# Kernel tuning notes

Hardware: AMD Instinct MI355X
Metric: run time of the kernel (lower is better)

## Reference

```python
import jax, jax.numpy as jnp
import numpy as np

ATT_PROP = 2  # config['att_prop']
NEG_BIAS = 1e23


def _bucket(d):
    # standard coref-style distance bucketing into 10 buckets
    d = jnp.abs(d)
    return jnp.where(d <= 4, d,
           jnp.where(d <= 7, 5,
           jnp.where(d <= 15, 6,
           jnp.where(d <= 31, 7,
           jnp.where(d <= 63, 8, 9))))).astype(jnp.int32)


def setup_inputs() -> dict:
    key = jax.random.key(0)
    ks = jax.random.split(key, 12)
    B, N, M, D, H = 2, 1024, 2048, 512, 64
    scale = 0.02  # init_weights_std

    update = jax.random.normal(ks[0], (B, N, D), jnp.float32)
    span_begin = jnp.sort(jax.random.randint(ks[1], (B, N), 0, 2000), axis=-1).astype(jnp.int32)
    span_end = (span_begin + jax.random.randint(ks[2], (B, N), 0, 10)).astype(jnp.int32)
    square_mask = jnp.ones((B, N, N), jnp.float32)
    cand_span_vecs = jax.random.normal(ks[3], (B, M, D), jnp.float32)
    # unique prune indices per batch (a pruned span maps to one candidate slot)
    prune_indices_hoi = jnp.stack([
        jnp.sort(jax.random.permutation(jax.random.fold_in(ks[4], b), M)[:N])
        for b in range(B)]).astype(jnp.int32)
    span_lengths = jnp.array([900, 1024], dtype=jnp.int32)

    W_left = jax.random.normal(ks[5], (D, H), jnp.float32) * scale
    W_right = jax.random.normal(ks[6], (D, H), jnp.float32) * scale
    b_h = jnp.zeros((H,), jnp.float32)
    dist_emb = jax.random.normal(ks[7], (10, H), jnp.float32) * scale
    v_out = jax.random.normal(ks[8], (H,), jnp.float32) * scale
    b_out = jnp.zeros((), jnp.float32)
    W_gate = jax.random.normal(ks[9], (2 * D, D), jnp.float32) * scale
    b_gate = jnp.zeros((D,), jnp.float32)

    return dict(update=update, square_mask=square_mask, cand_span_vecs=cand_span_vecs,
                span_begin=span_begin, span_end=span_end,
                prune_indices_hoi=prune_indices_hoi, span_lengths=span_lengths,
                W_left=W_left, W_right=W_right, b_h=b_h, dist_emb=dist_emb,
                v_out=v_out, b_out=b_out, W_gate=W_gate, b_gate=b_gate)


def reference(update, square_mask, cand_span_vecs, span_begin, span_end,
              prune_indices_hoi, span_lengths, W_left, W_right, b_h,
              dist_emb, v_out, b_out, W_gate, b_gate):
    B, N, D = update.shape
    # pairwise distance features are iteration-invariant: precompute once
    dist = dist_emb[_bucket(span_begin[:, :, None] - span_begin[:, None, :])]  # [B,N,N,H]
    bias = -(1.0 - square_mask) * NEG_BIAS  # [B,N,N]

    for _ in range(ATT_PROP):
        left = update @ W_left    # [B,N,H]
        right = update @ W_right  # [B,N,H]
        h = jax.nn.relu(left[:, :, None, :] + right[:, None, :, :] + dist + b_h)  # [B,N,N,H]
        scores = jnp.einsum('bijh,h->bij', h, v_out) + b_out  # [B,N,N]
        probs = jax.nn.softmax(scores + bias, axis=-1)
        ctxt = jnp.einsum('bij,bjd->bid', probs, update)  # [B,N,D]
        g = jax.nn.sigmoid(jnp.concatenate([update, ctxt], axis=-1) @ W_gate + b_gate)
        update = g * update + (1.0 - g) * ctxt

    # overwrite_spans_hoi: scatter first span_lengths[b] updated vectors back
    valid = jnp.arange(N) < span_lengths[:, None]  # [B,N]

    def scatter_one(cand, idx, upd, m):
        cur = cand[idx]  # [N,D]
        vals = jnp.where(m[:, None], upd, cur)  # invalid rows write back original
        return cand.at[idx].set(vals)

    cand_new = jax.vmap(scatter_one)(cand_span_vecs, prune_indices_hoi, update, valid)
    return cand_new, update
```

## Files before the change

### kernel.cpp

```cpp
#include <hip/hip_runtime.h>
#include <cstdint>

#define NB 2
#define NN 1024
#define MM 2048
#define DD 512
#define HH 64
#define ST 68
#define STB 72

typedef __attribute__((ext_vector_type(8))) short bf16x8;
typedef __attribute__((ext_vector_type(4))) float f32x4;

__device__ inline ushort f2bf(float x) {
  union { float f; uint32_t u; } v; v.f = x;
  uint32_t u = v.u;
  u += 0x7FFF + ((u >> 16) & 1);
  return (ushort)(u >> 16);
}
__device__ inline float bflo(uint32_t d) { return __uint_as_float(d << 16); }
__device__ inline float bfhi(uint32_t d) { return __uint_as_float(d & 0xFFFF0000u); }

#define GLDS(gp, lp) \
  __builtin_amdgcn_global_load_lds( \
      (const __attribute__((address_space(1))) void*)(gp), \
      (__attribute__((address_space(3))) void*)(lp), 16, 0, 0)

__global__ __launch_bounds__(256) void prep_kernel(
    const float* __restrict__ Wg, ushort* __restrict__ WgT,
    const float* __restrict__ update, ushort* __restrict__ Ubf0,
    ushort* __restrict__ UT, const float* __restrict__ cand,
    float* __restrict__ out, const float* __restrict__ Wl,
    const float* __restrict__ Wr, float* __restrict__ left,
    ushort* __restrict__ right_bf) {
  __shared__ __align__(16) char smem[16640];
  const int bid = blockIdx.x;
  const int tid = threadIdx.x;
  const int tx = tid & 15, ty = tid >> 4;

  if (bid < 384) {
    const float* in;
    ushort* out_row;
    ushort* out_T;
    int R, C, r0, c0;
    if (bid < 128) {
      in = Wg; out_row = nullptr; out_T = WgT;
      R = 2 * DD; C = DD; r0 = (bid >> 3) * 64; c0 = (bid & 7) * 64;
    } else {
      const int t = bid - 128, b = t >> 7, rem = t & 127;
      in = update + (size_t)b * NN * DD;
      out_row = Ubf0 + (size_t)b * NN * DD;
      out_T = UT + (size_t)b * DD * NN;
      R = NN; C = DD; r0 = (rem >> 3) * 64; c0 = (rem & 7) * 64;
    }
    float (*tile)[65] = (float(*)[65])smem;
#pragma unroll
    for (int p = 0; p < 4; ++p) {
      const int r = ty + p * 16;
      const float4 v = *(const float4*)&in[(size_t)(r0 + r) * C + c0 + tx * 4];
      tile[r][tx * 4 + 0] = v.x; tile[r][tx * 4 + 1] = v.y;
      tile[r][tx * 4 + 2] = v.z; tile[r][tx * 4 + 3] = v.w;
      if (out_row) {
        ushort4 o = make_ushort4(f2bf(v.x), f2bf(v.y), f2bf(v.z), f2bf(v.w));
        *(ushort4*)&out_row[(size_t)(r0 + r) * C + c0 + tx * 4] = o;
      }
    }
    __syncthreads();
#pragma unroll
    for (int p = 0; p < 4; ++p) {
      const int rr = ty + p * 16;
      ushort4 o;
      o.x = f2bf(tile[tx * 4 + 0][rr]);
      o.y = f2bf(tile[tx * 4 + 1][rr]);
      o.z = f2bf(tile[tx * 4 + 2][rr]);
      o.w = f2bf(tile[tx * 4 + 3][rr]);
      *(ushort4*)&out_T[(size_t)(c0 + rr) * R + r0 + tx * 4] = o;
    }
    __syncthreads();
  }

  {
    float (*u)[DD] = (float(*)[DD])smem;
    const float4* Uv = (const float4*)(update + (size_t)bid * 4 * DD);
    float4* uv = (float4*)&u[0][0];
#pragma unroll
    for (int t = 0; t < 2; ++t) uv[tid + t * 256] = Uv[tid + t * 256];
    __syncthreads();
    const int h = tid & 63;
    const int isR = (tid >> 6) & 1;
    const int rsel = tid >> 7;
    const float* __restrict__ W = isR ? Wr : Wl;
    float acc[2] = {0.f, 0.f};
    for (int k0 = 0; k0 < DD; k0 += 4) {
      float w0 = W[(k0 + 0) * HH + h];
      float w1 = W[(k0 + 1) * HH + h];
      float w2 = W[(k0 + 2) * HH + h];
      float w3 = W[(k0 + 3) * HH + h];
#pragma unroll
      for (int r = 0; r < 2; ++r) {
        float4 u4 = *(const float4*)&u[rsel + r * 2][k0];
        acc[r] = fmaf(u4.w, w3, fmaf(u4.z, w2, fmaf(u4.y, w1, fmaf(u4.x, w0, acc[r]))));
      }
    }
    if (isR) {
#pragma unroll
      for (int r = 0; r < 2; ++r)
        right_bf[(size_t)(bid * 4 + rsel + r * 2) * HH + h] = f2bf(acc[r]);
    } else {
#pragma unroll
      for (int r = 0; r < 2; ++r)
        left[(size_t)(bid * 4 + rsel + r * 2) * HH + h] = acc[r];
    }
  }

  {
    const float4* c4 = (const float4*)cand;
    float4* o4 = (float4*)out;
    for (int idx = bid * 256 + tid; idx < NB * MM * DD / 4; idx += 512 * 256)
      o4[idx] = c4[idx];
  }
}

__global__ __launch_bounds__(256) void lr_kernel(
    const float* __restrict__ U, const float* __restrict__ Wl,
    const float* __restrict__ Wr, float* __restrict__ left,
    ushort* __restrict__ right_bf) {
  __shared__ float u[4][DD];
  const int bid = blockIdx.x;
  const int tid = threadIdx.x;
  const float4* Uv = (const float4*)(U + (size_t)bid * 4 * DD);
  float4* uv = (float4*)&u[0][0];
#pragma unroll
  for (int t = 0; t < 2; ++t) uv[tid + t * 256] = Uv[tid + t * 256];
  __syncthreads();
  const int h = tid & 63;
  const int isR = (tid >> 6) & 1;
  const int rsel = tid >> 7;
  const float* __restrict__ W = isR ? Wr : Wl;
  float acc[2] = {0.f, 0.f};
  for (int k0 = 0; k0 < DD; k0 += 4) {
    float w0 = W[(k0 + 0) * HH + h];
    float w1 = W[(k0 + 1) * HH + h];
    float w2 = W[(k0 + 2) * HH + h];
    float w3 = W[(k0 + 3) * HH + h];
#pragma unroll
    for (int r = 0; r < 2; ++r) {
      float4 u4 = *(const float4*)&u[rsel + r * 2][k0];
      acc[r] = fmaf(u4.w, w3, fmaf(u4.z, w2, fmaf(u4.y, w1, fmaf(u4.x, w0, acc[r]))));
    }
  }
  if (isR) {
#pragma unroll
    for (int r = 0; r < 2; ++r)
      right_bf[(size_t)(bid * 4 + rsel + r * 2) * HH + h] = f2bf(acc[r]);
  } else {
#pragma unroll
    for (int r = 0; r < 2; ++r)
      left[(size_t)(bid * 4 + rsel + r * 2) * HH + h] = acc[r];
  }
}

__global__ __launch_bounds__(256) void score_softmax(
    const float* __restrict__ left, const ushort* __restrict__ right_bf,
    const int* __restrict__ span_begin, const float* __restrict__ mask,
    const float* __restrict__ dist_emb, const float* __restrict__ b_h,
    const float* __restrict__ v_out, ushort* __restrict__ probs_bf) {
  __shared__ ushort Rt[128][STB];
  __shared__ ushort LDb[4][10][STB];
  __shared__ float Dbh[10][ST];
  __shared__ float Lt[4][ST];
  __shared__ float Sc[4][NN];
  __shared__ int sbj[NN];
  const int b = blockIdx.y;
  const int r0 = blockIdx.x * 4;
  const int tid = threadIdx.x;
  const int wave = tid >> 6, lane = tid & 63;
  const int row = r0 + wave;

  for (int f = tid; f < 160; f += 256) {
    int bk = f >> 4, h4 = f & 15;
    float4 d = *(const float4*)&dist_emb[bk * HH + h4 * 4];
    float4 bh = *(const float4*)&b_h[h4 * 4];
    d.x += bh.x; d.y += bh.y; d.z += bh.z; d.w += bh.w;
    *(float4*)&Dbh[bk][h4 * 4] = d;
  }
  if (tid < 64) {
    int r = tid >> 4, h4 = tid & 15;
    *(float4*)&Lt[r][h4 * 4] =
        *(const float4*)&left[((size_t)b * NN + r0 + r) * HH + h4 * 4];
  }
  for (int t = tid; t < NN; t += 256) sbj[t] = span_begin[b * NN + t];
  __syncthreads();
  for (int f = tid; f < 2560; f += 256) {
    int i = f / 640;
    int rem = f - i * 640;
    int bk = rem >> 6, h = rem & 63;
    LDb[i][bk][h] = f2bf(Lt[i][h] + Dbh[bk][h]);
  }
  float4 vr[16];
#pragma unroll
  for (int hq = 0; hq < 16; ++hq) vr[hq] = *(const float4*)&v_out[hq * 4];
  const int my_sbi = span_begin[(size_t)b * NN + row];
  const float* maskrow = mask + ((size_t)b * NN + row) * NN;

#pragma unroll 1
  for (int c = 0; c < 8; ++c) {
    __syncthreads();
#pragma unroll
    for (int t = 0; t < 4; ++t) {
      const int f = tid + t * 256;
      const int r = f >> 3, u8 = f & 7;
      *(bf16x8*)&Rt[r][u8 * 8] =
          *(const bf16x8*)&right_bf[((size_t)b * NN + c * 128 + r) * HH + u8 * 8];
    }
    __syncthreads();
#pragma unroll 1
    for (int half = 0; half < 2; ++half) {
      const int j = c * 128 + half * 64 + lane;
      int d = sbj[j] - my_sbi;
      d = d < 0 ? -d : d;
      const int bk =
          d <= 4 ? d : (d <= 7 ? 5 : (d <= 15 ? 6 : (d <= 31 ? 7 : (d <= 63 ? 8 : 9))));
      const ushort* zp = &LDb[wave][bk][0];
      const ushort* rp = &Rt[half * 64 + lane][0];
      float acc0 = 0.f, acc1 = 0.f;
#pragma unroll
      for (int oct = 0; oct < 8; oct += 2) {
        {
          const uint4 zd = *(const uint4*)&zp[oct * 8];
          const uint4 rd = *(const uint4*)&rp[oct * 8];
          const float4 v0 = vr[2 * oct], v1 = vr[2 * oct + 1];
          acc0 = fmaf(fmaxf(bflo(zd.x) + bflo(rd.x), 0.f), v0.x, acc0);
          acc0 = fmaf(fmaxf(bfhi(zd.x) + bfhi(rd.x), 0.f), v0.y, acc0);
          acc0 = fmaf(fmaxf(bflo(zd.y) + bflo(rd.y), 0.f), v0.z, acc0);
          acc0 = fmaf(fmaxf(bfhi(zd.y) + bfhi(rd.y), 0.f), v0.w, acc0);
          acc0 = fmaf(fmaxf(bflo(zd.z) + bflo(rd.z), 0.f), v1.x, acc0);
          acc0 = fmaf(fmaxf(bfhi(zd.z) + bfhi(rd.z), 0.f), v1.y, acc0);
          acc0 = fmaf(fmaxf(bflo(zd.w) + bflo(rd.w), 0.f), v1.z, acc0);
          acc0 = fmaf(fmaxf(bfhi(zd.w) + bfhi(rd.w), 0.f), v1.w, acc0);
        }
        {
          const uint4 zd = *(const uint4*)&zp[(oct + 1) * 8];
          const uint4 rd = *(const uint4*)&rp[(oct + 1) * 8];
          const float4 v0 = vr[2 * oct + 2], v1 = vr[2 * oct + 3];
          acc1 = fmaf(fmaxf(bflo(zd.x) + bflo(rd.x), 0.f), v0.x, acc1);
          acc1 = fmaf(fmaxf(bfhi(zd.x) + bfhi(rd.x), 0.f), v0.y, acc1);
          acc1 = fmaf(fmaxf(bflo(zd.y) + bflo(rd.y), 0.f), v0.z, acc1);
          acc1 = fmaf(fmaxf(bfhi(zd.y) + bfhi(rd.y), 0.f), v0.w, acc1);
          acc1 = fmaf(fmaxf(bflo(zd.z) + bflo(rd.z), 0.f), v1.x, acc1);
          acc1 = fmaf(fmaxf(bfhi(zd.z) + bfhi(rd.z), 0.f), v1.y, acc1);
          acc1 = fmaf(fmaxf(bflo(zd.w) + bflo(rd.w), 0.f), v1.z, acc1);
          acc1 = fmaf(fmaxf(bfhi(zd.w) + bfhi(rd.w), 0.f), v1.w, acc1);
        }
      }
      const float mval = maskrow[j];
      Sc[wave][j] = (acc0 + acc1) - (1.0f - mval) * 1e23f;
    }
  }
  float mx = -3.0e38f;
#pragma unroll
  for (int c = 0; c < 16; ++c) mx = fmaxf(mx, Sc[wave][c * 64 + lane]);
#pragma unroll
  for (int off = 32; off; off >>= 1) mx = fmaxf(mx, __shfl_xor(mx, off));
  float sum = 0.f;
#pragma unroll
  for (int c = 0; c < 16; ++c) {
    const float e = __expf(Sc[wave][c * 64 + lane] - mx);
    Sc[wave][c * 64 + lane] = e;
    sum += e;
  }
#pragma unroll
  for (int off = 32; off; off >>= 1) sum += __shfl_xor(sum, off);
  const float inv = 1.0f / sum;
  ushort* prow = probs_bf + ((size_t)b * NN + row) * NN;
#pragma unroll
  for (int c = 0; c < 16; ++c)
    prow[c * 64 + lane] = f2bf(Sc[wave][c * 64 + lane] * inv);
}

__global__ __launch_bounds__(256) void gemm_ctxt_mfma(
    const ushort* __restrict__ Pbf, const ushort* __restrict__ UT,
    ushort* __restrict__ Cbf) {
  __shared__ ushort As[32 * 128];
  __shared__ ushort Bs[64 * 128];
  const int b = blockIdx.z;
  const int m0 = blockIdx.y * 32, n0 = blockIdx.x * 64;
  const int tid = threadIdx.x;
  const int lane = tid & 63, wave = tid >> 6;
  const int wm = (wave >> 1) * 16, wn = (wave & 1) * 32;
  const ushort* Ab = Pbf + (size_t)b * NN * NN;
  const ushort* Bb = UT + (size_t)b * DD * NN;
  f32x4 acc[2] = {};
  const int fm = lane & 15, quad = lane >> 4;
  for (int k0 = 0; k0 < NN; k0 += 128) {
#pragma unroll
    for (int t = 0; t < 2; ++t) {
      const int idx = tid + t * 256;
      const int r = idx >> 4, c16 = idx & 15;
      const int g = c16 ^ (r & 15);
      GLDS(Ab + (size_t)(m0 + r) * NN + k0 + g * 8, As + idx * 8);
    }
#pragma unroll
    for (int t = 0; t < 4; ++t) {
      const int idx = tid + t * 256;
      const int r = idx >> 4, c16 = idx & 15;
      const int g = c16 ^ (r & 15);
      GLDS(Bb + (size_t)(n0 + r) * NN + k0 + g * 8, Bs + idx * 8);
    }
    __syncthreads();
#pragma unroll
    for (int s = 0; s < 4; ++s) {
      bf16x8 af, bfr[2];
      {
        const int row = wm + fm;
        const int c16 = (s * 4 + quad) ^ (row & 15);
        af = *(const bf16x8*)&As[row * 128 + c16 * 8];
      }
#pragma unroll
      for (int tn = 0; tn < 2; ++tn) {
        const int row = wn + tn * 16 + fm;
        const int c16 = (s * 4 + quad) ^ (row & 15);
        bfr[tn] = *(const bf16x8*)&Bs[row * 128 + c16 * 8];
      }
#pragma unroll
      for (int tn = 0; tn < 2; ++tn)
        acc[tn] = __builtin_amdgcn_mfma_f32_16x16x32_bf16(af, bfr[tn], acc[tn], 0, 0, 0);
    }
    __syncthreads();
  }
#pragma unroll
  for (int tn = 0; tn < 2; ++tn) {
    const int col = n0 + wn + tn * 16 + fm;
#pragma unroll
    for (int r = 0; r < 4; ++r) {
      const int row = m0 + wm + quad * 4 + r;
      Cbf[(size_t)b * NN * DD + (size_t)row * DD + col] = f2bf(acc[tn][r]);
    }
  }
}

__global__ __launch_bounds__(256) void gemm_gate_mfma(
    const ushort* __restrict__ Ubf, const ushort* __restrict__ Cbf,
    const ushort* __restrict__ WgT, const float* __restrict__ bg,
    const float* __restrict__ Uf, float* __restrict__ Uout,
    ushort* __restrict__ UbfOut, ushort* __restrict__ UTOut,
    const int* __restrict__ prune, const int* __restrict__ span_len,
    float* __restrict__ out_cand, int final_it) {
  __shared__ ushort As[32 * 128];
  __shared__ ushort Bs[64 * 128];
  __shared__ ushort Tt[32][66];
  const int b = blockIdx.z;
  const int m0 = blockIdx.y * 32, n0 = blockIdx.x * 64;
  const int tid = threadIdx.x;
  const int lane = tid & 63, wave = tid >> 6;
  const int wm = (wave >> 1) * 16, wn = (wave & 1) * 32;
  f32x4 acc[2] = {};
  const int fm = lane & 15, quad = lane >> 4;
  for (int k0 = 0; k0 < 2 * DD; k0 += 128) {
    const ushort* Abase = (k0 < DD) ? (Ubf + (size_t)b * NN * DD)
                                    : (Cbf + (size_t)b * NN * DD);
    const int kc = k0 & (DD - 1);
#pragma unroll
    for (int t = 0; t < 2; ++t) {
      const int idx = tid + t * 256;
      const int r = idx >> 4, c16 = idx & 15;
      const int g = c16 ^ (r & 15);
      GLDS(Abase + (size_t)(m0 + r) * DD + kc + g * 8, As + idx * 8);
    }
#pragma unroll
    for (int t = 0; t < 4; ++t) {
      const int idx = tid + t * 256;
      const int r = idx >> 4, c16 = idx & 15;
      const int g = c16 ^ (r & 15);
      GLDS(WgT + (size_t)(n0 + r) * (2 * DD) + k0 + g * 8, Bs + idx * 8);
    }
    __syncthreads();
#pragma unroll
    for (int s = 0; s < 4; ++s) {
      bf16x8 af, bfr[2];
      {
        const int row = wm + fm;
        const int c16 = (s * 4 + quad) ^ (row & 15);
        af = *(const bf16x8*)&As[row * 128 + c16 * 8];
      }
#pragma unroll
      for (int tn = 0; tn < 2; ++tn) {
        const int row = wn + tn * 16 + fm;
        const int c16 = (s * 4 + quad) ^ (row & 15);
        bfr[tn] = *(const bf16x8*)&Bs[row * 128 + c16 * 8];
      }
#pragma unroll
      for (int tn = 0; tn < 2; ++tn)
        acc[tn] = __builtin_amdgcn_mfma_f32_16x16x32_bf16(af, bfr[tn], acc[tn], 0, 0, 0);
    }
    __syncthreads();
  }
  const int slen = span_len[b];
#pragma unroll
  for (int tn = 0; tn < 2; ++tn) {
    const int cl = wn + tn * 16 + fm;
    const int col = n0 + cl;
    const float bgv = bg[col];
#pragma unroll
    for (int r = 0; r < 4; ++r) {
      const int rl = wm + quad * 4 + r;
      const int row = m0 + rl;
      const size_t off = (size_t)b * NN * DD + (size_t)row * DD + col;
      const float g = 1.f / (1.f + __expf(-(acc[tn][r] + bgv)));
      const float cv = __uint_as_float(((uint32_t)Cbf[off]) << 16);
      const float o = g * Uf[off] + (1.f - g) * cv;
      Uout[off] = o;
      if (final_it) {
        if (row < slen) {
          const int dst = prune[b * NN + row];
          out_cand[((size_t)b * MM + dst) * DD + col] = o;
        }
      } else {
        const ushort ob = f2bf(o);
        UbfOut[off] = ob;
        Tt[rl][cl] = ob;
      }
    }
  }
  if (!final_it) {
    __syncthreads();
#pragma unroll
    for (int p = 0; p < 2; ++p) {
      const int cl = (tid >> 3) + p * 32;
      const int rl = (tid & 7) * 4;
      ushort4 o;
      o.x = Tt[rl + 0][cl]; o.y = Tt[rl + 1][cl];
      o.z = Tt[rl + 2][cl]; o.w = Tt[rl + 3][cl];
      *(ushort4*)&UTOut[((size_t)b * DD + n0 + cl) * NN + m0 + rl] = o;
    }
  }
}

extern "C" void kernel_launch(void* const* d_in, const int* in_sizes, int n_in,
                              void* d_out, int out_size, void* d_ws, size_t ws_size,
                              hipStream_t stream) {
  const float* update = (const float*)d_in[0];
  const float* mask = (const float*)d_in[1];
  const float* cand = (const float*)d_in[2];
  const int* span_begin = (const int*)d_in[3];
  const int* prune = (const int*)d_in[5];
  const int* span_len = (const int*)d_in[6];
  const float* Wl = (const float*)d_in[7];
  const float* Wr = (const float*)d_in[8];
  const float* b_h = (const float*)d_in[9];
  const float* dist_emb = (const float*)d_in[10];
  const float* v_out = (const float*)d_in[11];
  const float* Wg = (const float*)d_in[13];
  const float* b_gate = (const float*)d_in[14];

  char* w = (char*)d_ws;
  float* left = (float*)w;        w += (size_t)NB * NN * HH * 4;
  ushort* right_bf = (ushort*)w;  w += (size_t)NB * NN * HH * 2;
  ushort* probs_bf = (ushort*)w;  w += (size_t)NB * NN * NN * 2;
  ushort* ctxt_bf = (ushort*)w;   w += (size_t)NB * NN * DD * 2;
  float* upd1 = (float*)w;        w += (size_t)NB * NN * DD * 4;
  ushort* Ubf0 = (ushort*)w;      w += (size_t)NB * NN * DD * 2;
  ushort* Ubf1 = (ushort*)w;      w += (size_t)NB * NN * DD * 2;
  ushort* UT = (ushort*)w;        w += (size_t)NB * NN * DD * 2;
  ushort* WgT = (ushort*)w;       w += (size_t)2 * DD * DD * 2;

  float* out = (float*)d_out;
  float* out_upd = out + (size_t)NB * MM * DD;

  prep_kernel<<<512, 256, 0, stream>>>(Wg, WgT, update, Ubf0, UT, cand, out,
                                       Wl, Wr, left, right_bf);
  score_softmax<<<dim3(NN / 4, NB), 256, 0, stream>>>(
      left, right_bf, span_begin, mask, dist_emb, b_h, v_out, probs_bf);
  gemm_ctxt_mfma<<<dim3(8, 32, NB), 256, 0, stream>>>(probs_bf, UT, ctxt_bf);
  gemm_gate_mfma<<<dim3(8, 32, NB), 256, 0, stream>>>(
      Ubf0, ctxt_bf, WgT, b_gate, update, upd1, Ubf1, UT,
      prune, span_len, out, 0);
  lr_kernel<<<512, 256, 0, stream>>>(upd1, Wl, Wr, left, right_bf);
  score_softmax<<<dim3(NN / 4, NB), 256, 0, stream>>>(
      left, right_bf, span_begin, mask, dist_emb, b_h, v_out, probs_bf);
  gemm_ctxt_mfma<<<dim3(8, 32, NB), 256, 0, stream>>>(probs_bf, UT, ctxt_bf);
  gemm_gate_mfma<<<dim3(8, 32, NB), 256, 0, stream>>>(
      Ubf1, ctxt_bf, WgT, b_gate, upd1, out_upd, nullptr, nullptr,
      prune, span_len, out, 1);
}
```

Measured before the change: 222.0 us.

## Double-buffer shared tiles in score, ctxt and gate kernels to overlap loads

The score kernel now prefetches the next 128-row chunk of right_bf into registers while computing the current chunk, then writes it into a second LDS buffer. This removes one barrier per chunk, and the mask values are loaded up front. The ctxt and gate MFMA GEMMs use ping-pong LDS buffers so the async global-to-LDS copy of tile k+1 is issued before computing tile k, which also drops the trailing barrier. In exchange, LDS use doubles and register pressure rises, which may lower occupancy.

```diff
diff --git a/kernel.cpp b/kernel.cpp
--- a/kernel.cpp
+++ b/kernel.cpp
@@ -165,7 +165,7 @@
     const int* __restrict__ span_begin, const float* __restrict__ mask,
     const float* __restrict__ dist_emb, const float* __restrict__ b_h,
     const float* __restrict__ v_out, ushort* __restrict__ probs_bf) {
-  __shared__ ushort Rt[128][STB];
+  __shared__ ushort Rt[2][128][STB];
   __shared__ ushort LDb[4][10][STB];
   __shared__ float Dbh[10][ST];
   __shared__ float Lt[4][ST];
@@ -202,19 +202,35 @@
   for (int hq = 0; hq < 16; ++hq) vr[hq] = *(const float4*)&v_out[hq * 4];
   const int my_sbi = span_begin[(size_t)b * NN + row];
   const float* maskrow = mask + ((size_t)b * NN + row) * NN;
+  const ushort* rbase = right_bf + (size_t)b * NN * HH;
+
+  bf16x8 stg[4];
+#pragma unroll
+  for (int t = 0; t < 4; ++t) {
+    const int f = tid + t * 256;
+    stg[t] = *(const bf16x8*)&rbase[(size_t)(f >> 3) * HH + (f & 7) * 8];
+  }
+#pragma unroll
+  for (int t = 0; t < 4; ++t) {
+    const int f = tid + t * 256;
+    *(bf16x8*)&Rt[0][f >> 3][(f & 7) * 8] = stg[t];
+  }
 
 #pragma unroll 1
   for (int c = 0; c < 8; ++c) {
-    __syncthreads();
-#pragma unroll
-    for (int t = 0; t < 4; ++t) {
-      const int f = tid + t * 256;
-      const int r = f >> 3, u8 = f & 7;
-      *(bf16x8*)&Rt[r][u8 * 8] =
-          *(const bf16x8*)&right_bf[((size_t)b * NN + c * 128 + r) * HH + u8 * 8];
-    }
-    __syncthreads();
-#pragma unroll 1
+    if (c + 1 < 8) {
+#pragma unroll
+      for (int t = 0; t < 4; ++t) {
+        const int f = tid + t * 256;
+        stg[t] = *(const bf16x8*)&rbase[(size_t)((c + 1) * 128 + (f >> 3)) * HH +
+                                        (f & 7) * 8];
+      }
+    }
+    __syncthreads();
+    float mv[2];
+    mv[0] = maskrow[c * 128 + lane];
+    mv[1] = maskrow[c * 128 + 64 + lane];
+#pragma unroll
     for (int half = 0; half < 2; ++half) {
       const int j = c * 128 + half * 64 + lane;
       int d = sbj[j] - my_sbi;
@@ -222,7 +238,7 @@
       const int bk =
           d <= 4 ? d : (d <= 7 ? 5 : (d <= 15 ? 6 : (d <= 31 ? 7 : (d <= 63 ? 8 : 9))));
       const ushort* zp = &LDb[wave][bk][0];
-      const ushort* rp = &Rt[half * 64 + lane][0];
+      const ushort* rp = &Rt[c & 1][half * 64 + lane][0];
       float acc0 = 0.f, acc1 = 0.f;
 #pragma unroll
       for (int oct = 0; oct < 8; oct += 2) {
@@ -253,8 +269,14 @@
           acc1 = fmaf(fmaxf(bfhi(zd.w) + bfhi(rd.w), 0.f), v1.w, acc1);
         }
       }
-      const float mval = maskrow[j];
-      Sc[wave][j] = (acc0 + acc1) - (1.0f - mval) * 1e23f;
+      Sc[wave][j] = (acc0 + acc1) - (1.0f - mv[half]) * 1e23f;
+    }
+    if (c + 1 < 8) {
+#pragma unroll
+      for (int t = 0; t < 4; ++t) {
+        const int f = tid + t * 256;
+        *(bf16x8*)&Rt[(c + 1) & 1][f >> 3][(f & 7) * 8] = stg[t];
+      }
     }
   }
   float mx = -3.0e38f;
@@ -281,8 +303,8 @@
 __global__ __launch_bounds__(256) void gemm_ctxt_mfma(
     const ushort* __restrict__ Pbf, const ushort* __restrict__ UT,
     ushort* __restrict__ Cbf) {
-  __shared__ ushort As[32 * 128];
-  __shared__ ushort Bs[64 * 128];
+  __shared__ ushort As[2][32 * 128];
+  __shared__ ushort Bs[2][64 * 128];
   const int b = blockIdx.z;
   const int m0 = blockIdx.y * 32, n0 = blockIdx.x * 64;
   const int tid = threadIdx.x;
@@ -292,41 +314,47 @@
   const ushort* Bb = UT + (size_t)b * DD * NN;
   f32x4 acc[2] = {};
   const int fm = lane & 15, quad = lane >> 4;
-  for (int k0 = 0; k0 < NN; k0 += 128) {
-#pragma unroll
-    for (int t = 0; t < 2; ++t) {
-      const int idx = tid + t * 256;
-      const int r = idx >> 4, c16 = idx & 15;
-      const int g = c16 ^ (r & 15);
-      GLDS(Ab + (size_t)(m0 + r) * NN + k0 + g * 8, As + idx * 8);
-    }
-#pragma unroll
-    for (int t = 0; t < 4; ++t) {
-      const int idx = tid + t * 256;
-      const int r = idx >> 4, c16 = idx & 15;
-      const int g = c16 ^ (r & 15);
-      GLDS(Bb + (size_t)(n0 + r) * NN + k0 + g * 8, Bs + idx * 8);
-    }
-    __syncthreads();
+
+#define CTXT_STAGE(buf, kk)                                                  \
+  do {                                                                       \
+    _Pragma("unroll") for (int t = 0; t < 2; ++t) {                          \
+      const int idx = tid + t * 256;                                         \
+      const int r = idx >> 4, c16 = idx & 15;                                \
+      const int g = c16 ^ (r & 15);                                          \
+      GLDS(Ab + (size_t)(m0 + r) * NN + (kk) + g * 8, &As[buf][idx * 8]);    \
+    }                                                                        \
+    _Pragma("unroll") for (int t = 0; t < 4; ++t) {                          \
+      const int idx = tid + t * 256;                                         \
+      const int r = idx >> 4, c16 = idx & 15;                                \
+      const int g = c16 ^ (r & 15);                                          \
+      GLDS(Bb + (size_t)(n0 + r) * NN + (kk) + g * 8, &Bs[buf][idx * 8]);    \
+    }                                                                        \
+  } while (0)
+
+  CTXT_STAGE(0, 0);
+#pragma unroll 1
+  for (int k = 0; k < 8; ++k) {
+    __syncthreads();
+    if (k + 1 < 8) CTXT_STAGE((k + 1) & 1, (k + 1) * 128);
+    const int cur = k & 1;
 #pragma unroll
     for (int s = 0; s < 4; ++s) {
       bf16x8 af, bfr[2];
       {
         const int row = wm + fm;
         const int c16 = (s * 4 + quad) ^ (row & 15);
-        af = *(const bf16x8*)&As[row * 128 + c16 * 8];
+        af = *(const bf16x8*)&As[cur][row * 128 + c16 * 8];
       }
 #pragma unroll
       for (int tn = 0; tn < 2; ++tn) {
         const int row = wn + tn * 16 + fm;
         const int c16 = (s * 4 + quad) ^ (row & 15);
-        bfr[tn] = *(const bf16x8*)&Bs[row * 128 + c16 * 8];
+        bfr[tn] = *(const bf16x8*)&Bs[cur][row * 128 + c16 * 8];
       }
 #pragma unroll
       for (int tn = 0; tn < 2; ++tn)
         acc[tn] = __builtin_amdgcn_mfma_f32_16x16x32_bf16(af, bfr[tn], acc[tn], 0, 0, 0);
     }
-    __syncthreads();
   }
 #pragma unroll
   for (int tn = 0; tn < 2; ++tn) {
@@ -346,8 +374,8 @@
     ushort* __restrict__ UbfOut, ushort* __restrict__ UTOut,
     const int* __restrict__ prune, const int* __restrict__ span_len,
     float* __restrict__ out_cand, int final_it) {
-  __shared__ ushort As[32 * 128];
-  __shared__ ushort Bs[64 * 128];
+  __shared__ ushort As[2][32 * 128];
+  __shared__ ushort Bs[2][64 * 128];
   __shared__ ushort Tt[32][66];
   const int b = blockIdx.z;
   const int m0 = blockIdx.y * 32, n0 = blockIdx.x * 64;
@@ -356,44 +384,51 @@
   const int wm = (wave >> 1) * 16, wn = (wave & 1) * 32;
   f32x4 acc[2] = {};
   const int fm = lane & 15, quad = lane >> 4;
-  for (int k0 = 0; k0 < 2 * DD; k0 += 128) {
-    const ushort* Abase = (k0 < DD) ? (Ubf + (size_t)b * NN * DD)
-                                    : (Cbf + (size_t)b * NN * DD);
-    const int kc = k0 & (DD - 1);
-#pragma unroll
-    for (int t = 0; t < 2; ++t) {
-      const int idx = tid + t * 256;
-      const int r = idx >> 4, c16 = idx & 15;
-      const int g = c16 ^ (r & 15);
-      GLDS(Abase + (size_t)(m0 + r) * DD + kc + g * 8, As + idx * 8);
-    }
-#pragma unroll
-    for (int t = 0; t < 4; ++t) {
-      const int idx = tid + t * 256;
-      const int r = idx >> 4, c16 = idx & 15;
-      const int g = c16 ^ (r & 15);
-      GLDS(WgT + (size_t)(n0 + r) * (2 * DD) + k0 + g * 8, Bs + idx * 8);
-    }
-    __syncthreads();
+  const ushort* Au = Ubf + (size_t)b * NN * DD;
+  const ushort* Ac = Cbf + (size_t)b * NN * DD;
+
+#define GATE_STAGE(buf, kk)                                                  \
+  do {                                                                       \
+    const ushort* Abase = ((kk) < DD) ? Au : Ac;                             \
+    const int kc = (kk) & (DD - 1);                                          \
+    _Pragma("unroll") for (int t = 0; t < 2; ++t) {                          \
+      const int idx = tid + t * 256;                                         \
+      const int r = idx >> 4, c16 = idx & 15;                                \
+      const int g = c16 ^ (r & 15);                                          \
+      GLDS(Abase + (size_t)(m0 + r) * DD + kc + g * 8, &As[buf][idx * 8]);   \
+    }                                                                        \
+    _Pragma("unroll") for (int t = 0; t < 4; ++t) {                          \
+      const int idx = tid + t * 256;                                         \
+      const int r = idx >> 4, c16 = idx & 15;                                \
+      const int g = c16 ^ (r & 15);                                          \
+      GLDS(WgT + (size_t)(n0 + r) * (2 * DD) + (kk) + g * 8, &Bs[buf][idx * 8]); \
+    }                                                                        \
+  } while (0)
+
+  GATE_STAGE(0, 0);
+#pragma unroll 1
+  for (int k = 0; k < 8; ++k) {
+    __syncthreads();
+    if (k + 1 < 8) GATE_STAGE((k + 1) & 1, (k + 1) * 128);
+    const int cur = k & 1;
 #pragma unroll
     for (int s = 0; s < 4; ++s) {
       bf16x8 af, bfr[2];
       {
         const int row = wm + fm;
         const int c16 = (s * 4 + quad) ^ (row & 15);
-        af = *(const bf16x8*)&As[row * 128 + c16 * 8];
+        af = *(const bf16x8*)&As[cur][row * 128 + c16 * 8];
       }
 #pragma unroll
       for (int tn = 0; tn < 2; ++tn) {
         const int row = wn + tn * 16 + fm;
         const int c16 = (s * 4 + quad) ^ (row & 15);
-        bfr[tn] = *(const bf16x8*)&Bs[row * 128 + c16 * 8];
+        bfr[tn] = *(const bf16x8*)&Bs[cur][row * 128 + c16 * 8];
       }
 #pragma unroll
       for (int tn = 0; tn < 2; ++tn)
         acc[tn] = __builtin_amdgcn_mfma_f32_16x16x32_bf16(af, bfr[tn], acc[tn], 0, 0, 0);
     }
-    __syncthreads();
   }
   const int slen = span_len[b];
 #pragma unroll
```

Result: no change. 223.3 us (+0.6%).
